# Kernel optimization log

Measured on AMD Instinct MI355X. Metric: run time of the kernel, lower is better.

The kernel has to match this reference:

```python
import jax, jax.numpy as jnp
import numpy as np

EPS = 1e-12  # matches torch F.normalize eps


def setup_inputs() -> dict:
    key = jax.random.key(0)
    k1, k2, k3 = jax.random.split(key, 3)
    N, C, H, W, K = 16, 1024, 32, 32, 32
    x = jax.random.normal(k1, (N, C, H, W), dtype=jnp.float32)
    # 1x1 conv weight (K, C, 1, 1) stored as (K, C)
    conv_w = jax.random.normal(k2, (K, C), dtype=jnp.float32) * 0.02
    centroids = jax.random.uniform(k3, (K, C), dtype=jnp.float32)
    return {"x": x, "conv_w": conv_w, "centroids": centroids}


def _l2norm(v, axis):
    return v / jnp.maximum(jnp.linalg.norm(v, axis=axis, keepdims=True), EPS)


def reference(x, conv_w, centroids):
    N, C, H, W = x.shape
    K = centroids.shape[0]
    # normalize_input: L2 over channel dim
    x = _l2norm(x, axis=1)
    xf = x.reshape(N, C, H * W)                      # (N, C, P)
    # 1x1 conv == per-pixel matmul -> (N, K, P)
    logits = jnp.einsum('kc,ncp->nkp', conv_w, xf)
    a = jax.nn.softmax(logits, axis=1)               # softmax over clusters
    # sum_p a[n,k,p] * (x[n,:,p] - centroids[k,:])
    # == (a @ x^T) - (sum_p a) * centroids  (two GEMMs, no (N,K,C,P) blowup)
    vlad = jnp.einsum('nkp,ncp->nkc', a, xf) - a.sum(-1)[:, :, None] * centroids[None]
    vlad = _l2norm(vlad, axis=2)                     # intra-cluster L2 norm
    vlad = vlad.reshape(N, K * C)
    vlad = _l2norm(vlad, axis=1)                     # global L2 norm
    return vlad
```

## Files before the change

kernel.cpp:

```cpp
#include <hip/hip_runtime.h>

#define NB   16
#define CC   1024
#define PP   1024
#define KK   32
#define EPSF 1e-12f
#define NSLAB 8

typedef __attribute__((ext_vector_type(8))) short  bf16x8;
typedef __attribute__((ext_vector_type(4))) float  f32x4;

__device__ __forceinline__ float bf2f(unsigned short u) {
    union { unsigned int i; float f; } v; v.i = ((unsigned int)u) << 16; return v.f;
}
__device__ __forceinline__ unsigned short f2bf(float f) {
    union { float f; unsigned int i; } v; v.f = f;
    return (unsigned short)((v.i + 0x7fffu + ((v.i >> 16) & 1u)) >> 16);
}

template <typename T> struct IO;
template <> struct IO<float> {
    static __device__ __forceinline__ float ld(const float* p) { return *p; }
    static __device__ __forceinline__ f32x4 ld4(const float* p) { return *(const f32x4*)p; }
    static __device__ __forceinline__ void st4(float* p, f32x4 v) { *(f32x4*)p = v; }
};
template <> struct IO<unsigned short> {
    static __device__ __forceinline__ float ld(const unsigned short* p) { return bf2f(*p); }
    static __device__ __forceinline__ f32x4 ld4(const unsigned short* p) {
        const ushort4 u = *(const ushort4*)p;
        f32x4 r; r[0] = bf2f(u.x); r[1] = bf2f(u.y); r[2] = bf2f(u.z); r[3] = bf2f(u.w);
        return r;
    }
    static __device__ __forceinline__ void st4(unsigned short* p, f32x4 v) {
        ushort4 u;
        u.x = f2bf(v[0]); u.y = f2bf(v[1]); u.z = f2bf(v[2]); u.w = f2bf(v[3]);
        *(ushort4*)p = u;
    }
};

struct LogSmem {
    unsigned short xT[256][72];
    unsigned short W[32][136];
    float red[8][256];
};

template <typename T>
__device__ __forceinline__ void logits_body(const T* __restrict__ x,
                                            const T* __restrict__ w,
                                            LogSmem& sm,
                                            float* __restrict__ logits_p,
                                            float* __restrict__ ssq_p) {
    const int b = blockIdx.x, t = threadIdx.x;
    const int n = b >> 5, r = b & 31, s = r >> 2, pq = r & 3;
    const int c0 = s * 128, p0 = pq * 256;
    const int lane = t & 63, wvi = t >> 6;
    const int quad = lane >> 4, l15 = lane & 15;
    {
        const int k = t >> 3, coff = (t & 7) * 16;
        #pragma unroll
        for (int j = 0; j < 4; ++j) {
            const f32x4 v = IO<T>::ld4(&w[k * CC + c0 + coff + 4 * j]);
            ushort4 u;
            u.x = f2bf(v[0]); u.y = f2bf(v[1]); u.z = f2bf(v[2]); u.w = f2bf(v[3]);
            *(ushort4*)&sm.W[k][coff + 4 * j] = u;
        }
    }
    const int g  = t >> 5;
    const int po = (t & 31) * 8;
    const size_t xb = (size_t)n * CC * PP;
    float ssq_t[8] = {};
    f32x4 acc[2][4] = {};

    #pragma unroll
    for (int ch = 0; ch < 4; ++ch) {
        f32x4 vr[4][2];
        #pragma unroll
        for (int i = 0; i < 4; ++i) {
            const size_t row = xb + (size_t)(c0 + ch * 32 + g * 4 + i) * PP + p0 + po;
            vr[i][0] = IO<T>::ld4(&x[row]);
            vr[i][1] = IO<T>::ld4(&x[row + 4]);
        }
        __syncthreads();
        #pragma unroll
        for (int hj = 0; hj < 8; ++hj) {
            const int h = hj >> 2, j = hj & 3;
            ssq_t[hj] += vr[0][h][j] * vr[0][h][j] + vr[1][h][j] * vr[1][h][j]
                       + vr[2][h][j] * vr[2][h][j] + vr[3][h][j] * vr[3][h][j];
            ushort4 u;
            u.x = f2bf(vr[0][h][j]); u.y = f2bf(vr[1][h][j]);
            u.z = f2bf(vr[2][h][j]); u.w = f2bf(vr[3][h][j]);
            const int p_loc = po + hj;
            const int swz = ((p_loc >> 3) ^ (p_loc >> 5)) & 3;
            const int colg = (((g >> 1) ^ swz) * 8) + (g & 1) * 4;
            *(ushort4*)&sm.xT[p_loc][colg] = u;
        }
        __syncthreads();
        #pragma unroll
        for (int mt = 0; mt < 2; ++mt) {
            const bf16x8 av = *(const bf16x8*)&sm.W[mt * 16 + l15][ch * 32 + quad * 8];
            #pragma unroll
            for (int pt = 0; pt < 4; ++pt) {
                const int p_loc = wvi * 64 + pt * 16 + l15;
                const int swz = ((p_loc >> 3) ^ (p_loc >> 5)) & 3;
                const bf16x8 bv = *(const bf16x8*)&sm.xT[p_loc][(quad ^ swz) * 8];
                acc[mt][pt] = __builtin_amdgcn_mfma_f32_16x16x32_bf16(av, bv, acc[mt][pt], 0, 0, 0);
            }
        }
    }
    #pragma unroll
    for (int mt = 0; mt < 2; ++mt)
        #pragma unroll
        for (int pt = 0; pt < 4; ++pt)
            #pragma unroll
            for (int reg = 0; reg < 4; ++reg) {
                const int kk = mt * 16 + quad * 4 + reg;
                const int p  = p0 + wvi * 64 + pt * 16 + l15;
                logits_p[(((size_t)s * NB + n) * KK + kk) * PP + p] = acc[mt][pt][reg];
            }
    #pragma unroll
    for (int hj = 0; hj < 8; ++hj) sm.red[g][po + hj] = ssq_t[hj];
    __syncthreads();
    {
        float ss = 0.f;
        #pragma unroll
        for (int gg = 0; gg < 8; ++gg) ss += sm.red[gg][t];
        ssq_p[((size_t)s * NB + n) * PP + p0 + t] = ss;
    }
}

__global__ __launch_bounds__(256) void k_logits(const void* __restrict__ xv,
                                                const void* __restrict__ wv,
                                                int* __restrict__ flag,
                                                float* __restrict__ logits_p,
                                                float* __restrict__ ssq_p) {
    __shared__ LogSmem sm;
    __shared__ int s_bad;
    const int t = threadIdx.x;
    if (t == 0) s_bad = 0;
    __syncthreads();
    {
        const unsigned short* xu = (const unsigned short*)xv;
        int bad = 0;
        for (int i = t; i < 4096; i += 256)
            if (((xu[i] >> 7) & 0xFFu) > 0x9Fu) bad = 1;
        if (bad) atomicOr(&s_bad, 1);
    }
    __syncthreads();
    const int f = s_bad;
    if (blockIdx.x == 0 && t == 0) flag[0] = f;
    if (f) logits_body<float>((const float*)xv, (const float*)wv, sm, logits_p, ssq_p);
    else   logits_body<unsigned short>((const unsigned short*)xv, (const unsigned short*)wv,
                                       sm, logits_p, ssq_p);
}

__global__ __launch_bounds__(256) void k_soft(const float* __restrict__ logits_p,
                                              const float* __restrict__ ssq_p,
                                              float* __restrict__ rnorm_ws,
                                              unsigned short* __restrict__ attn_g,
                                              float* __restrict__ asum_p) {
    __shared__ float s_rn[32];
    __shared__ float s_as[32];
    const int b = blockIdx.x, t = threadIdx.x;
    const int n = b >> 5, ps = b & 31;
    const int p0 = ps * 32;
    if (t < 32) {
        float ss = 0.f;
        #pragma unroll
        for (int s = 0; s < NSLAB; ++s) ss += ssq_p[((size_t)s * NB + n) * PP + p0 + t];
        const float rr = 1.0f / fmaxf(sqrtf(ss), EPSF);
        s_rn[t] = rr;
        rnorm_ws[n * PP + p0 + t] = rr;
        s_as[t] = 0.f;
    }
    __syncthreads();
    const int pl = t >> 3, kg = (t & 7) * 4;
    const float rn = s_rn[pl];
    float l[4];
    #pragma unroll
    for (int j = 0; j < 4; ++j) {
        float a = 0.f;
        #pragma unroll
        for (int s = 0; s < NSLAB; ++s)
            a += logits_p[(((size_t)s * NB + n) * KK + kg + j) * PP + p0 + pl];
        l[j] = a * rn;
    }
    float mx = fmaxf(fmaxf(l[0], l[1]), fmaxf(l[2], l[3]));
    mx = fmaxf(mx, __shfl_xor(mx, 1, 64));
    mx = fmaxf(mx, __shfl_xor(mx, 2, 64));
    mx = fmaxf(mx, __shfl_xor(mx, 4, 64));
    float e[4], sum = 0.f;
    #pragma unroll
    for (int j = 0; j < 4; ++j) { e[j] = expf(l[j] - mx); sum += e[j]; }
    sum += __shfl_xor(sum, 1, 64);
    sum += __shfl_xor(sum, 2, 64);
    sum += __shfl_xor(sum, 4, 64);
    const float inv = 1.0f / sum;
    #pragma unroll
    for (int j = 0; j < 4; ++j) {
        const unsigned short uu = f2bf(e[j] * inv);
        attn_g[((size_t)n * KK + kg + j) * PP + p0 + pl] = uu;
        atomicAdd(&s_as[kg + j], bf2f(uu));
    }
    __syncthreads();
    if (t < 32) asum_p[(n * 32 + ps) * KK + t] = s_as[t];
}

struct VladSmem { float asum[32]; float ssq[32]; };

template <typename T>
__device__ __forceinline__ void vlad_body(const T* __restrict__ x,
                                          const T* __restrict__ cent, VladSmem& sm,
                                          const float* __restrict__ rnorm_ws,
                                          const unsigned short* __restrict__ attn_g,
                                          const float* __restrict__ asum_p,
                                          float* __restrict__ vlad,
                                          float* __restrict__ ssqnk_p) {
    const int b = blockIdx.x, t = threadIdx.x;
    const int n = b >> 5, ct = b & 31;
    const int lane = t & 63, wvi = t >> 6;
    const int quad = lane >> 4, l15 = lane & 15;
    const int mt = wvi & 1, nt = wvi >> 1;
    const int krow = mt * 16 + l15;
    const int crow = ct * 32 + nt * 16 + l15;
    if (t < 32) {
        float s = 0.f;
        #pragma unroll
        for (int ps = 0; ps < 32; ++ps) s += asum_p[(n * 32 + ps) * KK + t];
        sm.asum[t] = s;
        sm.ssq[t] = 0.f;
    }
    __syncthreads();
    const unsigned short* apq = attn_g + ((size_t)n * KK + krow) * PP + quad * 8;
    const T* xp = x + (size_t)n * CC * PP + (size_t)crow * PP + quad * 8;
    const float* rp = rnorm_ws + n * PP + quad * 8;
    f32x4 acc = {0.f, 0.f, 0.f, 0.f};
    bf16x8 avq[4]; f32x4 xq0[4], xq1[4], rq0[4], rq1[4];
    #pragma unroll
    for (int i = 0; i < 4; ++i) {
        const int o = i * 32;
        avq[i] = *(const bf16x8*)&apq[o];
        xq0[i] = IO<T>::ld4(&xp[o]); xq1[i] = IO<T>::ld4(&xp[o + 4]);
        rq0[i] = *(const f32x4*)&rp[o]; rq1[i] = *(const f32x4*)&rp[o + 4];
    }
    #pragma unroll
    for (int st = 0; st < 32; ++st) {
        const int sl = st & 3;
        bf16x8 bv;
        #pragma unroll
        for (int j = 0; j < 4; ++j) {
            bv[j]     = (short)f2bf(xq0[sl][j] * rq0[sl][j]);
            bv[4 + j] = (short)f2bf(xq1[sl][j] * rq1[sl][j]);
        }
        acc = __builtin_amdgcn_mfma_f32_16x16x32_bf16(avq[sl], bv, acc, 0, 0, 0);
        if (st + 4 < 32) {
            const int o = (st + 4) * 32;
            avq[sl] = *(const bf16x8*)&apq[o];
            xq0[sl] = IO<T>::ld4(&xp[o]); xq1[sl] = IO<T>::ld4(&xp[o + 4]);
            rq0[sl] = *(const f32x4*)&rp[o]; rq1[sl] = *(const f32x4*)&rp[o + 4];
        }
    }
    #pragma unroll
    for (int reg = 0; reg < 4; ++reg) {
        const int kk = mt * 16 + quad * 4 + reg;
        const float A = sm.asum[kk];
        const float v = acc[reg] - A * IO<T>::ld(&cent[kk * CC + crow]);
        vlad[((size_t)n * KK + kk) * CC + crow] = v;
        float sq = v * v;
        sq += __shfl_xor(sq, 1, 64);
        sq += __shfl_xor(sq, 2, 64);
        sq += __shfl_xor(sq, 4, 64);
        sq += __shfl_xor(sq, 8, 64);
        if (l15 == 0) atomicAdd(&sm.ssq[kk], sq);
    }
    __syncthreads();
    if (t < 32) ssqnk_p[(n * 32 + ct) * KK + t] = sm.ssq[t];
}

__global__ __launch_bounds__(256) void k_vlad(const void* __restrict__ xv,
                                              const void* __restrict__ centv,
                                              const int* __restrict__ flag,
                                              const float* __restrict__ rnorm_ws,
                                              const unsigned short* __restrict__ attn_g,
                                              const float* __restrict__ asum_p,
                                              float* __restrict__ vlad,
                                              float* __restrict__ ssqnk_p) {
    __shared__ VladSmem sm;
    if (*flag) vlad_body<float>((const float*)xv, (const float*)centv, sm, rnorm_ws,
                                attn_g, asum_p, vlad, ssqnk_p);
    else       vlad_body<unsigned short>((const unsigned short*)xv, (const unsigned short*)centv,
                                         sm, rnorm_ws, attn_g, asum_p, vlad, ssqnk_p);
}

struct OutSmem { float ssq[32]; float rint[32]; float rg; };

template <typename T>
__device__ __forceinline__ void out_body(const float* __restrict__ vlad,
                                         const float* __restrict__ ssqnk_p,
                                         OutSmem& sm, T* __restrict__ out) {
    const int b = blockIdx.x, t = threadIdx.x;
    const int n = b >> 5, k = b & 31;
    if (t < 32) {
        float s = 0.f;
        #pragma unroll
        for (int ct = 0; ct < 32; ++ct) s += ssqnk_p[(n * 32 + ct) * KK + t];
        sm.ssq[t] = s;
    }
    __syncthreads();
    if (t < 64) {
        const float s = (t < 32) ? sm.ssq[t] : 0.f;
        const float rr = 1.0f / fmaxf(sqrtf(s), EPSF);
        float gg = s * rr * rr;
        #pragma unroll
        for (int off = 32; off > 0; off >>= 1) gg += __shfl_down(gg, off, 64);
        if (t == 0) sm.rg = 1.0f / fmaxf(sqrtf(gg), EPSF);
        if (t < 32) sm.rint[t] = rr;
    }
    __syncthreads();
    const float f = sm.rint[k] * sm.rg;
    const size_t ob = ((size_t)n * KK + k) * CC + 4 * t;
    f32x4 v = *(const f32x4*)&vlad[ob];
    v[0] *= f; v[1] *= f; v[2] *= f; v[3] *= f;
    IO<T>::st4(&out[ob], v);
}

__global__ __launch_bounds__(256) void k_out(const float* __restrict__ vlad,
                                             const float* __restrict__ ssqnk_p,
                                             const int* __restrict__ flag,
                                             void* __restrict__ outv) {
    __shared__ OutSmem sm;
    if (*flag) out_body<float>(vlad, ssqnk_p, sm, (float*)outv);
    else       out_body<unsigned short>(vlad, ssqnk_p, sm, (unsigned short*)outv);
}

extern "C" void kernel_launch(void* const* d_in, const int* in_sizes, int n_in,
                              void* d_out, int out_size, void* d_ws, size_t ws_size,
                              hipStream_t stream) {
    const void* x    = d_in[0];
    const void* w    = d_in[1];
    const void* cent = d_in[2];

    float* ws        = (float*)d_ws;
    float* logits_p  = ws;
    float* ssq_p     = logits_p + (size_t)NSLAB * NB * KK * PP;
    float* rnorm_ws  = ssq_p + (size_t)NSLAB * NB * PP;
    float* asum_p    = rnorm_ws + NB * PP;
    float* ssqnk_p   = asum_p + NB * 32 * KK;
    float* vlad      = ssqnk_p + NB * 32 * KK;
    int*   flag      = (int*)(vlad + (size_t)NB * KK * CC);
    unsigned short* attn_g = (unsigned short*)(flag + 4);

    k_logits<<<NB * 32, 256, 0, stream>>>(x, w, flag, logits_p, ssq_p);
    k_soft<<<NB * 32, 256, 0, stream>>>(logits_p, ssq_p, rnorm_ws, attn_g, asum_p);
    k_vlad<<<NB * 32, 256, 0, stream>>>(x, cent, flag, rnorm_ws, attn_g, asum_p,
                                        vlad, ssqnk_p);
    k_out<<<NB * KK, 256, 0, stream>>>(vlad, ssqnk_p, flag, d_out);
}
```

Before: 140.4 us.

## Fuse logits and softmax into one kernel over full channel range per pixel tile

Replaces the channel-split logits kernel and the separate softmax kernel with a single kernel where each block loops over all 1024 channels for a 64-pixel tile. The kernel double-buffers LDS and uses a lighter barrier. It computes the L2 norm, logits, softmax, attention and per-tile attention sums in place. This removes the fp32 partial-logit workspace round trip and one kernel launch. In exchange the grid shrinks to 256 blocks with a long serial channel loop, which may lower parallelism and latency hiding.

```diff
diff --git a/kernel.cpp b/kernel.cpp
--- a/kernel.cpp
+++ b/kernel.cpp
@@ -5,7 +5,6 @@
 #define PP   1024
 #define KK   32
 #define EPSF 1e-12f
-#define NSLAB 8
 
 typedef __attribute__((ext_vector_type(8))) short  bf16x8;
 typedef __attribute__((ext_vector_type(4))) float  f32x4;
@@ -38,102 +37,142 @@
     }
 };
 
-struct LogSmem {
-    unsigned short xT[256][72];
-    unsigned short W[32][136];
-    float red[8][256];
+__device__ __forceinline__ void wg_sync_fast() {
+    asm volatile("s_waitcnt lgkmcnt(0)" ::: "memory");
+    __builtin_amdgcn_s_barrier();
+    asm volatile("" ::: "memory");
+}
+
+struct __align__(16) AttnSmem {
+    unsigned short xT[2][64][72];
+    unsigned short Wl[2][32][72];
+    float red[16][64];
+    float rn[64];
 };
 
 template <typename T>
-__device__ __forceinline__ void logits_body(const T* __restrict__ x,
-                                            const T* __restrict__ w,
-                                            LogSmem& sm,
-                                            float* __restrict__ logits_p,
-                                            float* __restrict__ ssq_p) {
+__device__ __forceinline__ void attn_body(const T* __restrict__ x,
+                                          const T* __restrict__ w,
+                                          AttnSmem& sm,
+                                          float* __restrict__ rnorm_ws,
+                                          unsigned short* __restrict__ attn_g,
+                                          float* __restrict__ asum_p) {
     const int b = blockIdx.x, t = threadIdx.x;
-    const int n = b >> 5, r = b & 31, s = r >> 2, pq = r & 3;
-    const int c0 = s * 128, p0 = pq * 256;
-    const int lane = t & 63, wvi = t >> 6;
+    const int n = b >> 4, pt = b & 15, p0 = pt * 64;
+    const int lane = t & 63, wv = t >> 6;
     const int quad = lane >> 4, l15 = lane & 15;
+    const int i = t >> 4;
+    const int j = t & 15;
+    const int wk = t >> 3;
+    const int wcoff = (t & 7) * 8;
+    const size_t xb = (size_t)n * CC * PP + p0;
+
+    float ssq_t[4] = {0.f, 0.f, 0.f, 0.f};
+    f32x4 acc0 = {0.f, 0.f, 0.f, 0.f}, acc1 = {0.f, 0.f, 0.f, 0.f};
+
+    f32x4 xr[4]; f32x4 wr[2];
+    #pragma unroll
+    for (int r = 0; r < 4; ++r)
+        xr[r] = IO<T>::ld4(&x[xb + (size_t)(4 * i + r) * PP + 4 * j]);
+    wr[0] = IO<T>::ld4(&w[wk * CC + wcoff]);
+    wr[1] = IO<T>::ld4(&w[wk * CC + wcoff + 4]);
+
+    #pragma unroll
+    for (int ch = 0; ch < 16; ++ch) {
+        const int buf = ch & 1;
+        #pragma unroll
+        for (int jj = 0; jj < 4; ++jj) {
+            ssq_t[jj] += xr[0][jj] * xr[0][jj] + xr[1][jj] * xr[1][jj]
+                       + xr[2][jj] * xr[2][jj] + xr[3][jj] * xr[3][jj];
+            ushort4 u;
+            u.x = f2bf(xr[0][jj]); u.y = f2bf(xr[1][jj]);
+            u.z = f2bf(xr[2][jj]); u.w = f2bf(xr[3][jj]);
+            *(ushort4*)&sm.xT[buf][4 * j + jj][4 * i] = u;
+        }
+        {
+            ushort4 u0, u1;
+            u0.x = f2bf(wr[0][0]); u0.y = f2bf(wr[0][1]);
+            u0.z = f2bf(wr[0][2]); u0.w = f2bf(wr[0][3]);
+            u1.x = f2bf(wr[1][0]); u1.y = f2bf(wr[1][1]);
+            u1.z = f2bf(wr[1][2]); u1.w = f2bf(wr[1][3]);
+            *(ushort4*)&sm.Wl[buf][wk][wcoff]     = u0;
+            *(ushort4*)&sm.Wl[buf][wk][wcoff + 4] = u1;
+        }
+        if (ch < 15) {
+            const int c0 = (ch + 1) * 64;
+            #pragma unroll
+            for (int r = 0; r < 4; ++r)
+                xr[r] = IO<T>::ld4(&x[xb + (size_t)(c0 + 4 * i + r) * PP + 4 * j]);
+            wr[0] = IO<T>::ld4(&w[wk * CC + c0 + wcoff]);
+            wr[1] = IO<T>::ld4(&w[wk * CC + c0 + wcoff + 4]);
+        }
+        wg_sync_fast();
+        #pragma unroll
+        for (int ks = 0; ks < 2; ++ks) {
+            const bf16x8 bv  = *(const bf16x8*)&sm.xT[buf][wv * 16 + l15][ks * 32 + quad * 8];
+            const bf16x8 a0  = *(const bf16x8*)&sm.Wl[buf][l15][ks * 32 + quad * 8];
+            const bf16x8 a1  = *(const bf16x8*)&sm.Wl[buf][16 + l15][ks * 32 + quad * 8];
+            acc0 = __builtin_amdgcn_mfma_f32_16x16x32_bf16(a0, bv, acc0, 0, 0, 0);
+            acc1 = __builtin_amdgcn_mfma_f32_16x16x32_bf16(a1, bv, acc1, 0, 0, 0);
+        }
+    }
+    #pragma unroll
+    for (int jj = 0; jj < 4; ++jj) sm.red[i][4 * j + jj] = ssq_t[jj];
+    __syncthreads();
+    if (t < 64) {
+        float ss = 0.f;
+        #pragma unroll
+        for (int g = 0; g < 16; ++g) ss += sm.red[g][t];
+        const float rr = 1.0f / fmaxf(sqrtf(ss), EPSF);
+        sm.rn[t] = rr;
+        rnorm_ws[n * PP + p0 + t] = rr;
+    }
+    __syncthreads();
     {
-        const int k = t >> 3, coff = (t & 7) * 16;
-        #pragma unroll
-        for (int j = 0; j < 4; ++j) {
-            const f32x4 v = IO<T>::ld4(&w[k * CC + c0 + coff + 4 * j]);
-            ushort4 u;
-            u.x = f2bf(v[0]); u.y = f2bf(v[1]); u.z = f2bf(v[2]); u.w = f2bf(v[3]);
-            *(ushort4*)&sm.W[k][coff + 4 * j] = u;
-        }
-    }
-    const int g  = t >> 5;
-    const int po = (t & 31) * 8;
-    const size_t xb = (size_t)n * CC * PP;
-    float ssq_t[8] = {};
-    f32x4 acc[2][4] = {};
-
-    #pragma unroll
-    for (int ch = 0; ch < 4; ++ch) {
-        f32x4 vr[4][2];
-        #pragma unroll
-        for (int i = 0; i < 4; ++i) {
-            const size_t row = xb + (size_t)(c0 + ch * 32 + g * 4 + i) * PP + p0 + po;
-            vr[i][0] = IO<T>::ld4(&x[row]);
-            vr[i][1] = IO<T>::ld4(&x[row + 4]);
-        }
-        __syncthreads();
-        #pragma unroll
-        for (int hj = 0; hj < 8; ++hj) {
-            const int h = hj >> 2, j = hj & 3;
-            ssq_t[hj] += vr[0][h][j] * vr[0][h][j] + vr[1][h][j] * vr[1][h][j]
-                       + vr[2][h][j] * vr[2][h][j] + vr[3][h][j] * vr[3][h][j];
-            ushort4 u;
-            u.x = f2bf(vr[0][h][j]); u.y = f2bf(vr[1][h][j]);
-            u.z = f2bf(vr[2][h][j]); u.w = f2bf(vr[3][h][j]);
-            const int p_loc = po + hj;
-            const int swz = ((p_loc >> 3) ^ (p_loc >> 5)) & 3;
-            const int colg = (((g >> 1) ^ swz) * 8) + (g & 1) * 4;
-            *(ushort4*)&sm.xT[p_loc][colg] = u;
-        }
-        __syncthreads();
-        #pragma unroll
-        for (int mt = 0; mt < 2; ++mt) {
-            const bf16x8 av = *(const bf16x8*)&sm.W[mt * 16 + l15][ch * 32 + quad * 8];
-            #pragma unroll
-            for (int pt = 0; pt < 4; ++pt) {
-                const int p_loc = wvi * 64 + pt * 16 + l15;
-                const int swz = ((p_loc >> 3) ^ (p_loc >> 5)) & 3;
-                const bf16x8 bv = *(const bf16x8*)&sm.xT[p_loc][(quad ^ swz) * 8];
-                acc[mt][pt] = __builtin_amdgcn_mfma_f32_16x16x32_bf16(av, bv, acc[mt][pt], 0, 0, 0);
-            }
-        }
-    }
-    #pragma unroll
-    for (int mt = 0; mt < 2; ++mt)
-        #pragma unroll
-        for (int pt = 0; pt < 4; ++pt)
-            #pragma unroll
-            for (int reg = 0; reg < 4; ++reg) {
-                const int kk = mt * 16 + quad * 4 + reg;
-                const int p  = p0 + wvi * 64 + pt * 16 + l15;
-                logits_p[(((size_t)s * NB + n) * KK + kk) * PP + p] = acc[mt][pt][reg];
-            }
-    #pragma unroll
-    for (int hj = 0; hj < 8; ++hj) sm.red[g][po + hj] = ssq_t[hj];
+        const float rr = sm.rn[wv * 16 + l15];
+        float l[8];
+        #pragma unroll
+        for (int reg = 0; reg < 4; ++reg) { l[reg] = acc0[reg] * rr; l[4 + reg] = acc1[reg] * rr; }
+        float mx = l[0];
+        #pragma unroll
+        for (int q = 1; q < 8; ++q) mx = fmaxf(mx, l[q]);
+        mx = fmaxf(mx, __shfl_xor(mx, 16, 64));
+        mx = fmaxf(mx, __shfl_xor(mx, 32, 64));
+        float e[8], sum = 0.f;
+        #pragma unroll
+        for (int q = 0; q < 8; ++q) { e[q] = expf(l[q] - mx); sum += e[q]; }
+        sum += __shfl_xor(sum, 16, 64);
+        sum += __shfl_xor(sum, 32, 64);
+        const float inv = 1.0f / sum;
+        #pragma unroll
+        for (int reg = 0; reg < 4; ++reg) {
+            sm.Wl[0][quad * 4 + reg][wv * 16 + l15]      = f2bf(e[reg] * inv);
+            sm.Wl[0][16 + quad * 4 + reg][wv * 16 + l15] = f2bf(e[4 + reg] * inv);
+        }
+    }
     __syncthreads();
     {
-        float ss = 0.f;
-        #pragma unroll
-        for (int gg = 0; gg < 8; ++gg) ss += sm.red[gg][t];
-        ssq_p[((size_t)s * NB + n) * PP + p0 + t] = ss;
-    }
-}
-
-__global__ __launch_bounds__(256) void k_logits(const void* __restrict__ xv,
-                                                const void* __restrict__ wv,
-                                                int* __restrict__ flag,
-                                                float* __restrict__ logits_p,
-                                                float* __restrict__ ssq_p) {
-    __shared__ LogSmem sm;
+        const int k = t >> 3, po = (t & 7) * 8;
+        const ushort4 u0 = *(const ushort4*)&sm.Wl[0][k][po];
+        const ushort4 u1 = *(const ushort4*)&sm.Wl[0][k][po + 4];
+        *(ushort4*)&attn_g[((size_t)n * KK + k) * PP + p0 + po]     = u0;
+        *(ushort4*)&attn_g[((size_t)n * KK + k) * PP + p0 + po + 4] = u1;
+        float s = bf2f(u0.x) + bf2f(u0.y) + bf2f(u0.z) + bf2f(u0.w)
+                + bf2f(u1.x) + bf2f(u1.y) + bf2f(u1.z) + bf2f(u1.w);
+        s += __shfl_xor(s, 1, 64);
+        s += __shfl_xor(s, 2, 64);
+        s += __shfl_xor(s, 4, 64);
+        if ((t & 7) == 0) asum_p[(n * 16 + pt) * KK + k] = s;
+    }
+}
+
+__global__ __launch_bounds__(256) void k_attn(const void* __restrict__ xv,
+                                              const void* __restrict__ wv,
+                                              int* __restrict__ flag,
+                                              float* __restrict__ rnorm_ws,
+                                              unsigned short* __restrict__ attn_g,
+                                              float* __restrict__ asum_p) {
+    __shared__ AttnSmem sm;
     __shared__ int s_bad;
     const int t = threadIdx.x;
     if (t == 0) s_bad = 0;
@@ -141,68 +180,16 @@
     {
         const unsigned short* xu = (const unsigned short*)xv;
         int bad = 0;
-        for (int i = t; i < 4096; i += 256)
-            if (((xu[i] >> 7) & 0xFFu) > 0x9Fu) bad = 1;
+        for (int ii = t; ii < 4096; ii += 256)
+            if (((xu[ii] >> 7) & 0xFFu) > 0x9Fu) bad = 1;
         if (bad) atomicOr(&s_bad, 1);
     }
     __syncthreads();
     const int f = s_bad;
     if (blockIdx.x == 0 && t == 0) flag[0] = f;
-    if (f) logits_body<float>((const float*)xv, (const float*)wv, sm, logits_p, ssq_p);
-    else   logits_body<unsigned short>((const unsigned short*)xv, (const unsigned short*)wv,
-                                       sm, logits_p, ssq_p);
-}
-
-__global__ __launch_bounds__(256) void k_soft(const float* __restrict__ logits_p,
-                                              const float* __restrict__ ssq_p,
-                                              float* __restrict__ rnorm_ws,
-                                              unsigned short* __restrict__ attn_g,
-                                              float* __restrict__ asum_p) {
-    __shared__ float s_rn[32];
-    __shared__ float s_as[32];
-    const int b = blockIdx.x, t = threadIdx.x;
-    const int n = b >> 5, ps = b & 31;
-    const int p0 = ps * 32;
-    if (t < 32) {
-        float ss = 0.f;
-        #pragma unroll
-        for (int s = 0; s < NSLAB; ++s) ss += ssq_p[((size_t)s * NB + n) * PP + p0 + t];
-        const float rr = 1.0f / fmaxf(sqrtf(ss), EPSF);
-        s_rn[t] = rr;
-        rnorm_ws[n * PP + p0 + t] = rr;
-        s_as[t] = 0.f;
-    }
-    __syncthreads();
-    const int pl = t >> 3, kg = (t & 7) * 4;
-    const float rn = s_rn[pl];
-    float l[4];
-    #pragma unroll
-    for (int j = 0; j < 4; ++j) {
-        float a = 0.f;
-        #pragma unroll
-        for (int s = 0; s < NSLAB; ++s)
-            a += logits_p[(((size_t)s * NB + n) * KK + kg + j) * PP + p0 + pl];
-        l[j] = a * rn;
-    }
-    float mx = fmaxf(fmaxf(l[0], l[1]), fmaxf(l[2], l[3]));
-    mx = fmaxf(mx, __shfl_xor(mx, 1, 64));
-    mx = fmaxf(mx, __shfl_xor(mx, 2, 64));
-    mx = fmaxf(mx, __shfl_xor(mx, 4, 64));
-    float e[4], sum = 0.f;
-    #pragma unroll
-    for (int j = 0; j < 4; ++j) { e[j] = expf(l[j] - mx); sum += e[j]; }
-    sum += __shfl_xor(sum, 1, 64);
-    sum += __shfl_xor(sum, 2, 64);
-    sum += __shfl_xor(sum, 4, 64);
-    const float inv = 1.0f / sum;
-    #pragma unroll
-    for (int j = 0; j < 4; ++j) {
-        const unsigned short uu = f2bf(e[j] * inv);
-        attn_g[((size_t)n * KK + kg + j) * PP + p0 + pl] = uu;
-        atomicAdd(&s_as[kg + j], bf2f(uu));
-    }
-    __syncthreads();
-    if (t < 32) asum_p[(n * 32 + ps) * KK + t] = s_as[t];
+    if (f) attn_body<float>((const float*)xv, (const float*)wv, sm, rnorm_ws, attn_g, asum_p);
+    else   attn_body<unsigned short>((const unsigned short*)xv, (const unsigned short*)wv,
+                                     sm, rnorm_ws, attn_g, asum_p);
 }
 
 struct VladSmem { float asum[32]; float ssq[32]; };
@@ -225,7 +212,7 @@
     if (t < 32) {
         float s = 0.f;
         #pragma unroll
-        for (int ps = 0; ps < 32; ++ps) s += asum_p[(n * 32 + ps) * KK + t];
+        for (int ps = 0; ps < 16; ++ps) s += asum_p[(n * 16 + ps) * KK + t];
         sm.asum[t] = s;
         sm.ssq[t] = 0.f;
     }
@@ -236,20 +223,20 @@
     f32x4 acc = {0.f, 0.f, 0.f, 0.f};
     bf16x8 avq[4]; f32x4 xq0[4], xq1[4], rq0[4], rq1[4];
     #pragma unroll
-    for (int i = 0; i < 4; ++i) {
-        const int o = i * 32;
-        avq[i] = *(const bf16x8*)&apq[o];
-        xq0[i] = IO<T>::ld4(&xp[o]); xq1[i] = IO<T>::ld4(&xp[o + 4]);
-        rq0[i] = *(const f32x4*)&rp[o]; rq1[i] = *(const f32x4*)&rp[o + 4];
+    for (int ii = 0; ii < 4; ++ii) {
+        const int o = ii * 32;
+        avq[ii] = *(const bf16x8*)&apq[o];
+        xq0[ii] = IO<T>::ld4(&xp[o]); xq1[ii] = IO<T>::ld4(&xp[o + 4]);
+        rq0[ii] = *(const f32x4*)&rp[o]; rq1[ii] = *(const f32x4*)&rp[o + 4];
     }
     #pragma unroll
     for (int st = 0; st < 32; ++st) {
         const int sl = st & 3;
         bf16x8 bv;
         #pragma unroll
-        for (int j = 0; j < 4; ++j) {
-            bv[j]     = (short)f2bf(xq0[sl][j] * rq0[sl][j]);
-            bv[4 + j] = (short)f2bf(xq1[sl][j] * rq1[sl][j]);
+        for (int jj = 0; jj < 4; ++jj) {
+            bv[jj]     = (short)f2bf(xq0[sl][jj] * rq0[sl][jj]);
+            bv[4 + jj] = (short)f2bf(xq1[sl][jj] * rq1[sl][jj]);
         }
         acc = __builtin_amdgcn_mfma_f32_16x16x32_bf16(avq[sl], bv, acc, 0, 0, 0);
         if (st + 4 < 32) {
@@ -339,18 +326,15 @@
     const void* w    = d_in[1];
     const void* cent = d_in[2];
 
-    float* ws        = (float*)d_ws;
-    float* logits_p  = ws;
-    float* ssq_p     = logits_p + (size_t)NSLAB * NB * KK * PP;
-    float* rnorm_ws  = ssq_p + (size_t)NSLAB * NB * PP;
-    float* asum_p    = rnorm_ws + NB * PP;
-    float* ssqnk_p   = asum_p + NB * 32 * KK;
-    float* vlad      = ssqnk_p + NB * 32 * KK;
-    int*   flag      = (int*)(vlad + (size_t)NB * KK * CC);
+    float* ws       = (float*)d_ws;
+    float* rnorm_ws = ws;
+    float* asum_p   = rnorm_ws + NB * PP;
+    float* ssqnk_p  = asum_p + NB * 16 * KK;
+    float* vlad     = ssqnk_p + NB * 32 * KK;
+    int*   flag     = (int*)(vlad + (size_t)NB * KK * CC);
     unsigned short* attn_g = (unsigned short*)(flag + 4);
 
-    k_logits<<<NB * 32, 256, 0, stream>>>(x, w, flag, logits_p, ssq_p);
-    k_soft<<<NB * 32, 256, 0, stream>>>(logits_p, ssq_p, rnorm_ws, attn_g, asum_p);
+    k_attn<<<NB * 16, 256, 0, stream>>>(x, w, flag, rnorm_ws, attn_g, asum_p);
     k_vlad<<<NB * 32, 256, 0, stream>>>(x, cent, flag, rnorm_ws, attn_g, asum_p,
                                         vlad, ssqnk_p);
     k_out<<<NB * KK, 256, 0, stream>>>(vlad, ssqnk_p, flag, d_out);
```

Result: faster. 133.0 us (-5.3%).
